# Kernel tuning notes

Measured on AMD Instinct MI355X. Metric: run time of the kernel, lower is better.

The kernel has to match this reference:

```python
import jax, jax.numpy as jnp
import numpy as np

N, E, DIM, H = 50000, 800000, 128, 8
HD = DIM // H  # head dim = 16
EPS = 1e-5


def setup_inputs() -> dict:
    key = jax.random.key(0)
    ks = jax.random.split(key, 12)
    s = 1.0 / np.sqrt(DIM)
    inp = {
        "h": jax.random.normal(ks[0], (N, DIM), jnp.float32),
        "src": jax.random.randint(ks[1], (E,), 0, N, jnp.int32),
        "dst": jax.random.randint(ks[2], (E,), 0, N, jnp.int32),
        "Wq": jax.random.normal(ks[3], (DIM, DIM), jnp.float32) * s,
        "Wk": jax.random.normal(ks[4], (DIM, DIM), jnp.float32) * s,
        "Wv": jax.random.normal(ks[5], (DIM, DIM), jnp.float32) * s,
        "Wo": jax.random.normal(ks[6], (DIM, DIM), jnp.float32) * s,
        "bo": jnp.zeros((DIM,), jnp.float32),
        "bn1_g": jnp.ones((DIM,), jnp.float32),
        "bn1_b": jnp.zeros((DIM,), jnp.float32),
        "bn2_g": jnp.ones((DIM,), jnp.float32),
        "bn2_b": jnp.zeros((DIM,), jnp.float32),
        "W1": jax.random.normal(ks[7], (DIM, 2 * DIM), jnp.float32) * s,
        "b1": jnp.zeros((2 * DIM,), jnp.float32),
        "W2": jax.random.normal(ks[8], (2 * DIM, DIM), jnp.float32) * (1.0 / np.sqrt(2 * DIM)),
        "b2": jnp.zeros((DIM,), jnp.float32),
    }
    return inp


def _batch_norm(x, g, b):
    # BatchNorm1d in training mode: biased batch statistics over the node axis
    mean = jnp.mean(x, axis=0)
    var = jnp.mean((x - mean) ** 2, axis=0)
    return (x - mean) * jax.lax.rsqrt(var + EPS) * g + b


def reference(h, src, dst, Wq, Wk, Wv, Wo, bo, bn1_g, bn1_b, bn2_g, bn2_b, W1, b1, W2, b2):
    n = h.shape[0]
    h_in1 = h
    hn = _batch_norm(h, bn1_g, bn1_b)

    # multi-head graph attention
    Q = (hn @ Wq).reshape(n, H, HD)
    K = (hn @ Wk).reshape(n, H, HD)
    V = (hn @ Wv).reshape(n, H, HD)

    # edge score: sum_d K[src]*Q[dst] / sqrt(HD), clamped to [-5, 5] -> [E, H]
    score = jnp.einsum('ehd,ehd->eh', K[src], Q[dst]) / np.sqrt(HD)
    score = jnp.clip(score, -5.0, 5.0)

    # edge_softmax: normalize over incoming edges of each destination node
    smax = jax.ops.segment_max(score, dst, num_segments=n)  # [N, H]
    a = jnp.exp(score - smax[dst])
    asum = jax.ops.segment_sum(a, dst, num_segments=n)  # [N, H]
    a = a / asum[dst]

    # weighted scatter-sum aggregation of V
    m = V[src] * a[:, :, None]  # [E, H, HD]
    wV = jax.ops.segment_sum(m, dst, num_segments=n).reshape(n, DIM)

    h2 = wV @ Wo + bo
    h2 = h_in1 + h2
    h_in2 = h2
    h3 = _batch_norm(h2, bn2_g, bn2_b)
    h3 = jax.nn.relu(h3 @ W1 + b1) @ W2 + b2
    return h_in2 + h3
```

## Files before the change

### kernel.cpp

```cpp
#include <hip/hip_runtime.h>
#include <hip/hip_bf16.h>

#define NDIM 128
#define NHEAD 8
#define EPSV 1e-5f

#if defined(__has_builtin)
#  if __has_builtin(__builtin_amdgcn_cvt_pk_fp8_f32) && __has_builtin(__builtin_amdgcn_cvt_pk_f32_fp8)
#    define HAVE_FP8 1
#  else
#    define HAVE_FP8 0
#  endif
#else
#  define HAVE_FP8 0
#endif

typedef unsigned short u16;
typedef unsigned char u8;
using bf16x8 = __attribute__((ext_vector_type(8))) short;
using f32x4  = __attribute__((ext_vector_type(4))) float;
using f32x2  = __attribute__((ext_vector_type(2))) float;
using us8    = __attribute__((ext_vector_type(8))) unsigned short;
using us4    = __attribute__((ext_vector_type(4))) unsigned short;

__device__ __forceinline__ u16 f2b(float x){
  union { float f; unsigned u; } v; v.f = x;
  unsigned r = v.u + 0x7FFFu + ((v.u >> 16) & 1u);
  return (u16)(r >> 16);
}
__device__ __forceinline__ float b2f(u16 u){
  union { unsigned u; float f; } v; v.u = ((unsigned)u) << 16; return v.f;
}
__device__ __forceinline__ float blo(unsigned u){
  union { unsigned u; float f; } v; v.u = u << 16; return v.f;
}
__device__ __forceinline__ float bhi(unsigned u){
  union { unsigned u; float f; } v; v.u = u & 0xFFFF0000u; return v.f;
}
__device__ __forceinline__ f32x2 b2f2(unsigned u){
  f32x2 r; r.x = blo(u); r.y = bhi(u); return r;
}

template<int NT, int MT, int KS, int WTLD, int XSTR>
__device__ __forceinline__ void gemm_tiles(const u16* X, const u16* __restrict__ WT,
                                           int lr, int kg, int colbase, f32x4 (&acc)[NT][MT]){
  #pragma unroll
  for (int ks = 0; ks < KS; ks++){
    bf16x8 a[MT];
    #pragma unroll
    for (int m = 0; m < MT; m++)
      a[m] = *(const bf16x8*)(X + (size_t)(m*16 + lr)*XSTR + ks*32 + kg*8);
    #pragma unroll
    for (int n = 0; n < NT; n++){
      int col = colbase + n*16 + lr;
      bf16x8 b = *(const bf16x8*)(WT + (size_t)col*WTLD + ks*32 + kg*8);
      #pragma unroll
      for (int m = 0; m < MT; m++)
        acc[n][m] = __builtin_amdgcn_mfma_f32_16x16x32_bf16(a[m], b, acc[n][m], 0, 0, 0);
    }
  }
}

__device__ __forceinline__ void wconv_tile(const float* __restrict__ W, u16* __restrict__ WT,
                                           int rows, int cols, int tr, int tc, int t){
  __shared__ u16 T[64][66];
  int r0 = tr*64, c0 = tc*64;
  int r = t >> 2, cq = (t & 3) * 16;
  const float* src = W + (size_t)(r0 + r)*cols + c0 + cq;
  #pragma unroll
  for (int j = 0; j < 4; j++){
    float4 v = *(const float4*)(src + 4*j);
    us4 o; o.x = f2b(v.x); o.y = f2b(v.y); o.z = f2b(v.z); o.w = f2b(v.w);
    *(us4*)&T[r][cq + 4*j] = o;
  }
  __syncthreads();
  int c = t >> 2, rq = (t & 3) * 16;
  us8 o0, o1;
  #pragma unroll
  for (int j = 0; j < 8; j++){ o0[j] = T[rq + j][c]; o1[j] = T[rq + 8 + j][c]; }
  u16* dstp = WT + (size_t)(c0 + c)*rows + r0 + rq;
  *(us8*)dstp = o0;
  *(us8*)(dstp + 8) = o1;
}

__global__ __launch_bounds__(256) void k_pro(
    const float* __restrict__ Wq, const float* __restrict__ Wk, const float* __restrict__ Wv,
    const float* __restrict__ Wo, const float* __restrict__ W1, const float* __restrict__ W2,
    u16* __restrict__ wtq, u16* __restrict__ wtk, u16* __restrict__ wtv,
    u16* __restrict__ wto, u16* __restrict__ wt1, u16* __restrict__ wt2,
    const float* __restrict__ h, float* __restrict__ part1,
    const int* __restrict__ dst, int* __restrict__ cntT,
    int nBn, int N, int E, int B, int C){
  __shared__ f32x4 lsS[256], lsQ[256];
  __shared__ int hist[256];
  int b = blockIdx.x, t = threadIdx.x;
  if (b < nBn){
    int qd = t & 31, rl = t >> 5;
    int r0 = b * 128;
    f32x4 s = {0.f,0.f,0.f,0.f}, sq = {0.f,0.f,0.f,0.f};
    for (int r = rl; r < 128; r += 8){
      int row = r0 + r;
      if (row < N){
        f32x4 v = *(const f32x4*)(h + (size_t)row*NDIM + qd*4);
        s += v; sq += v*v;
      }
    }
    lsS[t] = s; lsQ[t] = sq; __syncthreads();
    if (rl < 4){ lsS[t] += lsS[t+128]; lsQ[t] += lsQ[t+128]; } __syncthreads();
    if (rl < 2){ lsS[t] += lsS[t+64];  lsQ[t] += lsQ[t+64];  } __syncthreads();
    if (rl == 0){
      f32x4 S  = lsS[t] + lsS[t+32];
      f32x4 Qv = lsQ[t] + lsQ[t+32];
      *(f32x4*)&part1[(size_t)b*256 + qd*4]       = S;
      *(f32x4*)&part1[(size_t)b*256 + 128 + qd*4] = Qv;
    }
    return;
  }
  b -= nBn;
  if (b < 16){
    const float* Ws[4] = {Wq, Wk, Wv, Wo};
    u16* Ts[4] = {wtq, wtk, wtv, wto};
    int wi = b >> 2, ti = b & 3;
    wconv_tile(Ws[wi], Ts[wi], 128, 128, ti >> 1, ti & 1, t);
    return;
  }
  if (b < 24){
    int ti = b - 16;
    wconv_tile(W1, wt1, 128, 256, ti >> 2, ti & 3, t);
    return;
  }
  if (b < 32){
    int ti = b - 24;
    wconv_tile(W2, wt2, 256, 128, ti & 3, ti >> 2, t);
    return;
  }
  int ci = b - 32;
  if (ci >= C) return;
  hist[t] = 0; __syncthreads();
  int e0 = ci * 4096;
  #pragma unroll
  for (int j = 0; j < 16; j++){
    int e = e0 + t + j*256;
    if (e < E) atomicAdd(&hist[dst[e] >> 8], 1);
  }
  __syncthreads();
  if (t < B) cntT[t*C + ci] = hist[t];
}

__device__ __forceinline__ float reduce_part(const float* __restrict__ part, int nP, int t){
  float a0 = 0.f, a1 = 0.f, a2 = 0.f, a3 = 0.f;
  int i = 0;
  for (; i + 4 <= nP; i += 4){
    a0 += part[(size_t)(i+0)*256 + t];
    a1 += part[(size_t)(i+1)*256 + t];
    a2 += part[(size_t)(i+2)*256 + t];
    a3 += part[(size_t)(i+3)*256 + t];
  }
  for (; i < nP; i++) a0 += part[(size_t)i*256 + t];
  return (a0 + a1) + (a2 + a3);
}

__global__ __launch_bounds__(256) void k_bnf_scan(
    const float* __restrict__ part1, int nBn,
    const float* __restrict__ g, const float* __restrict__ b_,
    float* __restrict__ scsh, int N,
    const int* __restrict__ in, int* __restrict__ bsum, int len){
  __shared__ int ls[256];
  __shared__ float sm[256];
  int t = threadIdx.x, b = blockIdx.x;
  if (b == 0){
    sm[t] = reduce_part(part1, nBn, t);
    __syncthreads();
    if (t < 128){
      float mean = sm[t] / (float)N;
      float var  = sm[128+t] / (float)N - mean*mean;
      float rstd = rsqrtf(var + EPSV);
      float sc = g[t] * rstd;
      scsh[t] = sc; scsh[128+t] = b_[t] - mean*sc;
    }
    return;
  }
  b -= 1;
  int i = b*256 + t;
  ls[t] = (i < len) ? in[i] : 0; __syncthreads();
  for (int off = 128; off > 0; off >>= 1){
    if (t < off) ls[t] += ls[t + off];
    __syncthreads();
  }
  if (t == 0) bsum[b] = ls[0];
}

__global__ __launch_bounds__(256) void k_bn_final(const float* __restrict__ sets,
                                                  const float* __restrict__ g, const float* __restrict__ b,
                                                  float* __restrict__ scsh, int N){
  __shared__ float sm[256];
  int t = threadIdx.x;
  sm[t] = reduce_part(sets, 64, t);
  __syncthreads();
  if (t < 128){
    float mean = sm[t] / (float)N;
    float var  = sm[128+t] / (float)N - mean*mean;
    float rstd = rsqrtf(var + EPSV);
    float sc = g[t] * rstd;
    scsh[t] = sc; scsh[128+t] = b[t] - mean*sc;
  }
}

__global__ __launch_bounds__(256) void k_scan_top(int* __restrict__ bsum, int nb, int* __restrict__ rowptr, int N, int E){
  __shared__ int ls[256];
  int t = threadIdx.x;
  int v = (t < nb) ? bsum[t] : 0; ls[t] = v; __syncthreads();
  for (int off = 1; off < 256; off <<= 1){
    int add = (t >= off) ? ls[t - off] : 0;
    __syncthreads();
    ls[t] += add;
    __syncthreads();
  }
  if (t < nb) bsum[t] = ls[t] - v;
  if (t == 0) rowptr[N] = E;
}

__global__ __launch_bounds__(256) void k_scan_down(const int* __restrict__ in, const int* __restrict__ bsum,
                                                   int* __restrict__ outp, int len){
  __shared__ int ls[256];
  int t = threadIdx.x; int i = blockIdx.x*256 + t;
  int v = (i < len) ? in[i] : 0; ls[t] = v; __syncthreads();
  for (int off = 1; off < 256; off <<= 1){
    int add = (t >= off) ? ls[t - off] : 0;
    __syncthreads();
    ls[t] += add;
    __syncthreads();
  }
  if (i < len) outp[i] = ls[t] - v + bsum[blockIdx.x];
}

__global__ __launch_bounds__(256) void k_finesort(const int2* __restrict__ ebuf, const int* __restrict__ scn,
                                                  int* __restrict__ rowptr, int* __restrict__ csr_src,
                                                  int B, int C, int N, int E){
  __shared__ int ls[256], cur[256];
  int b = blockIdx.x, t = threadIdx.x;
  int base = scn[b*C];
  int end  = (b == B-1) ? E : scn[(b+1)*C];
  int lo = b << 8;
  cur[t] = 0; __syncthreads();
  for (int e = base + t; e < end; e += 256) atomicAdd(&cur[ebuf[e].x - lo], 1);
  __syncthreads();
  int v = cur[t]; ls[t] = v; __syncthreads();
  for (int off = 1; off < 256; off <<= 1){
    int add = (t >= off) ? ls[t - off] : 0;
    __syncthreads();
    ls[t] += add;
    __syncthreads();
  }
  int excl = ls[t] - v;
  __syncthreads();
  cur[t] = excl;
  if (lo + t < N) rowptr[lo + t] = base + excl;
  __syncthreads();
  for (int e = base + t; e < end; e += 256){
    int2 p = ebuf[e];
    int slot = base + atomicAdd(&cur[p.x - lo], 1);
    csr_src[slot] = p.y;
  }
}

__global__ __launch_bounds__(256) void k_qkv_bucket(
    const float* __restrict__ h, const float* __restrict__ scsh,
    const u16* __restrict__ WTq, const u16* __restrict__ WTk, const u16* __restrict__ WTv,
    u16* __restrict__ Q, u16* __restrict__ K, u16* __restrict__ V, int N,
    const int* __restrict__ src, const int* __restrict__ dst,
    const int* __restrict__ scn, int2* __restrict__ ebuf, int B, int C, int E){
  __shared__ u16 hn[32][136];
  __shared__ u16 ob[32][136];
  __shared__ int off[256];
  int b = blockIdx.x, t = threadIdx.x;
  if (b < C){
    off[t] = (t < B) ? scn[t*C + b] : 0;
    __syncthreads();
    int e0 = b * 4096;
    #pragma unroll
    for (int j = 0; j < 16; j++){
      int e = e0 + t + j*256;
      if (e < E){
        int d = dst[e], s = src[e];
        int slot = atomicAdd(&off[d >> 8], 1);
        ebuf[slot] = make_int2(d, s);
      }
    }
    return;
  }
  int r0 = (b - C) * 32;
  int row = t >> 3, c0 = (t & 7) * 16;
  {
    int rr = r0 + row;
    #pragma unroll
    for (int j = 0; j < 4; j++){
      int c = c0 + 4*j;
      float4 v = make_float4(0.f,0.f,0.f,0.f);
      if (rr < N) v = *(const float4*)(h + (size_t)rr*NDIM + c);
      us4 o;
      o.x = f2b(v.x * scsh[c]   + scsh[128+c]);
      o.y = f2b(v.y * scsh[c+1] + scsh[129+c]);
      o.z = f2b(v.z * scsh[c+2] + scsh[130+c]);
      o.w = f2b(v.w * scsh[c+3] + scsh[131+c]);
      *(us4*)&hn[row][c] = o;
    }
  }
  __syncthreads();
  int lane = t & 63, w = t >> 6;
  int lr = lane & 15, kg = lane >> 4;
  f32x4 zero = {0.f,0.f,0.f,0.f};

  #define DO_PASS(WT, OUT, FIRST) { \
    f32x4 acc[2][2]; \
    _Pragma("unroll") for (int n = 0; n < 2; n++) _Pragma("unroll") for (int m = 0; m < 2; m++) acc[n][m] = zero; \
    gemm_tiles<2,2,4,128,136>(&hn[0][0], WT, lr, kg, w*32, acc); \
    if (!FIRST) __syncthreads(); \
    _Pragma("unroll") for (int n = 0; n < 2; n++){ \
      int col = w*32 + n*16 + lr; \
      _Pragma("unroll") for (int m = 0; m < 2; m++) \
        _Pragma("unroll") for (int r = 0; r < 4; r++) \
          ob[m*16 + kg*4 + r][col] = f2b(acc[n][m][r]); \
    } \
    __syncthreads(); \
    if (r0 + row < N){ \
      u16* dp = OUT + (size_t)(r0 + row)*NDIM + c0; \
      *(us8*)dp       = *(const us8*)&ob[row][c0]; \
      *(us8*)(dp + 8) = *(const us8*)&ob[row][c0 + 8]; \
    } }

  DO_PASS(WTq, Q, true)

  {
    f32x4 acc[2][2];
    #pragma unroll
    for (int n = 0; n < 2; n++)
      #pragma unroll
      for (int m = 0; m < 2; m++) acc[n][m] = zero;
    gemm_tiles<2,2,4,128,136>(&hn[0][0], WTk, lr, kg, w*32, acc);
    __syncthreads();
    #pragma unroll
    for (int n = 0; n < 2; n++){
      int col = w*32 + n*16 + lr;
      #pragma unroll
      for (int m = 0; m < 2; m++)
        #pragma unroll
        for (int r = 0; r < 4; r++)
          ob[m*16 + kg*4 + r][col] = f2b(acc[n][m][r]);
    }
    __syncthreads();
    if (r0 + row < N){
#if HAVE_FP8
      u8* dp = (u8*)K + (size_t)(r0 + row)*NDIM + c0;
      unsigned wd[4];
      #pragma unroll
      for (int j = 0; j < 2; j++){
        us8 v = *(const us8*)&ob[row][c0 + 8*j];
        int w0 = __builtin_amdgcn_cvt_pk_fp8_f32(b2f(v[0]), b2f(v[1]), 0, false);
        w0     = __builtin_amdgcn_cvt_pk_fp8_f32(b2f(v[2]), b2f(v[3]), w0, true);
        int w1 = __builtin_amdgcn_cvt_pk_fp8_f32(b2f(v[4]), b2f(v[5]), 0, false);
        w1     = __builtin_amdgcn_cvt_pk_fp8_f32(b2f(v[6]), b2f(v[7]), w1, true);
        wd[2*j] = (unsigned)w0; wd[2*j+1] = (unsigned)w1;
      }
      *(uint4*)dp = make_uint4(wd[0], wd[1], wd[2], wd[3]);
#else
      u16* dp = K + (size_t)(r0 + row)*NDIM + c0;
      *(us8*)dp       = *(const us8*)&ob[row][c0];
      *(us8*)(dp + 8) = *(const us8*)&ob[row][c0 + 8];
#endif
    }
  }

  DO_PASS(WTv, V, false)
  #undef DO_PASS
}

__global__ __launch_bounds__(256) void k_sagg(const int* __restrict__ rowptr, const int* __restrict__ csr_src,
                                              const u16* __restrict__ Q, const u16* __restrict__ K,
                                              const u16* __restrict__ V, u16* __restrict__ wV, int N){
  __shared__ float wx[4][64];
  int w = threadIdx.x >> 6, l = threadIdx.x & 63;
  int n = blockIdx.x*4 + w;
  if (n >= N) return;
  int j8 = l >> 3, hh = l & 7, d0 = l * 2;

  f32x2 qf[8];
  {
    const unsigned* qp = (const unsigned*)(Q + (size_t)n*NDIM + hh*16);
    #pragma unroll
    for (int t = 0; t < 8; t++){
      unsigned u = qp[t];
      qf[t].x = blo(u) * 0.25f;
      qf[t].y = bhi(u) * 0.25f;
    }
  }

  int e0 = rowptr[n], e1 = rowptr[n+1];
  int i0 = __builtin_amdgcn_readfirstlane(e0);
  int deg = e1 - e0;
  int nw  = deg >> 3;
  int rem = deg & 7;

  float ssum_l = 0.f;
  f32x2 a01 = {0.f, 0.f};

#if HAVE_FP8
  const u8* Kb = (const u8*)K;
  uint4 kA, kB;
  #define KLOAD(dst_, sidx) dst_ = *(const uint4*)(Kb + (size_t)(sidx)*NDIM + (hh << 4));
  #define KDOTP(p, kk) { \
    f32x2 p2 = {0.f, 0.f}; \
    p2 += qf[0] * __builtin_amdgcn_cvt_pk_f32_fp8((int)kk.x, false); \
    p2 += qf[1] * __builtin_amdgcn_cvt_pk_f32_fp8((int)kk.x, true); \
    p2 += qf[2] * __builtin_amdgcn_cvt_pk_f32_fp8((int)kk.y, false); \
    p2 += qf[3] * __builtin_amdgcn_cvt_pk_f32_fp8((int)kk.y, true); \
    p2 += qf[4] * __builtin_amdgcn_cvt_pk_f32_fp8((int)kk.z, false); \
    p2 += qf[5] * __builtin_amdgcn_cvt_pk_f32_fp8((int)kk.z, true); \
    p2 += qf[6] * __builtin_amdgcn_cvt_pk_f32_fp8((int)kk.w, false); \
    p2 += qf[7] * __builtin_amdgcn_cvt_pk_f32_fp8((int)kk.w, true); \
    p = p2.x + p2.y; }
#else
  struct krow { uint4 lo, hi; };
  krow kA, kB;
  #define KLOAD(dst_, sidx) { \
    const uint4* kp_ = (const uint4*)(K + (size_t)(sidx)*NDIM + hh*16); \
    dst_.lo = kp_[0]; dst_.hi = kp_[1]; }
  #define KDOTP(p, kk) { \
    f32x2 p2 = {0.f, 0.f}; \
    p2 += qf[0] * b2f2(kk.lo.x); p2 += qf[1] * b2f2(kk.lo.y); \
    p2 += qf[2] * b2f2(kk.lo.z); p2 += qf[3] * b2f2(kk.lo.w); \
    p2 += qf[4] * b2f2(kk.hi.x); p2 += qf[5] * b2f2(kk.hi.y); \
    p2 += qf[6] * b2f2(kk.hi.z); p2 += qf[7] * b2f2(kk.hi.w); \
    p = p2.x + p2.y; }
#endif

  unsigned vvA[8], vvB[8];

  if (nw >= 1){
    int s0=csr_src[i0+0], s1=csr_src[i0+1], s2=csr_src[i0+2], s3=csr_src[i0+3];
    int s4=csr_src[i0+4], s5=csr_src[i0+5], s6=csr_src[i0+6], s7=csr_src[i0+7];
    vvA[0] = *(const unsigned*)(V + (size_t)s0*NDIM + d0);
    vvA[1] = *(const unsigned*)(V + (size_t)s1*NDIM + d0);
    vvA[2] = *(const unsigned*)(V + (size_t)s2*NDIM + d0);
    vvA[3] = *(const unsigned*)(V + (size_t)s3*NDIM + d0);
    vvA[4] = *(const unsigned*)(V + (size_t)s4*NDIM + d0);
    vvA[5] = *(const unsigned*)(V + (size_t)s5*NDIM + d0);
    vvA[6] = *(const unsigned*)(V + (size_t)s6*NDIM + d0);
    vvA[7] = *(const unsigned*)(V + (size_t)s7*NDIM + d0);
    int sidx = csr_src[e0 + j8];
    KLOAD(kA, sidx)
  }

  for (int wi = 0; wi < nw; wi++){
    if (wi + 1 < nw){
      int ib = i0 + wi*8 + 8;
      int s0=csr_src[ib+0], s1=csr_src[ib+1], s2=csr_src[ib+2], s3=csr_src[ib+3];
      int s4=csr_src[ib+4], s5=csr_src[ib+5], s6=csr_src[ib+6], s7=csr_src[ib+7];
      vvB[0] = *(const unsigned*)(V + (size_t)s0*NDIM + d0);
      vvB[1] = *(const unsigned*)(V + (size_t)s1*NDIM + d0);
      vvB[2] = *(const unsigned*)(V + (size_t)s2*NDIM + d0);
      vvB[3] = *(const unsigned*)(V + (size_t)s3*NDIM + d0);
      vvB[4] = *(const unsigned*)(V + (size_t)s4*NDIM + d0);
      vvB[5] = *(const unsigned*)(V + (size_t)s5*NDIM + d0);
      vvB[6] = *(const unsigned*)(V + (size_t)s6*NDIM + d0);
      vvB[7] = *(const unsigned*)(V + (size_t)s7*NDIM + d0);
      int sidx = csr_src[e0 + wi*8 + 8 + j8];
      KLOAD(kB, sidx)
    }
    float p;
    KDOTP(p, kA)
    p = fminf(5.f, fmaxf(-5.f, p));
    float wgt = __expf(p);
    ssum_l += wgt;
    wx[w][hh*8 + j8] = wgt;
    float4 wa = *(const float4*)&wx[w][j8*8];
    float4 wb = *(const float4*)&wx[w][j8*8 + 4];
    a01 += b2f2(vvA[0]) * wa.x;
    a01 += b2f2(vvA[1]) * wa.y;
    a01 += b2f2(vvA[2]) * wa.z;
    a01 += b2f2(vvA[3]) * wa.w;
    a01 += b2f2(vvA[4]) * wb.x;
    a01 += b2f2(vvA[5]) * wb.y;
    a01 += b2f2(vvA[6]) * wb.z;
    a01 += b2f2(vvA[7]) * wb.w;
    if (wi + 1 < nw){
      #pragma unroll
      for (int j = 0; j < 8; j++) vvA[j] = vvB[j];
      kA = kB;
    }
  }

  if (rem > 0){
    int i0t = i0 + nw*8;
    int s[8];
    #pragma unroll
    for (int j = 0; j < 8; j++) s[j] = csr_src[i0t + (j < rem ? j : 0)];
    unsigned vv[8];
    #pragma unroll
    for (int j = 0; j < 8; j++) vv[j] = *(const unsigned*)(V + (size_t)s[j]*NDIM + d0);
    int sidx = csr_src[i0t + (j8 < rem ? j8 : 0)];
#if HAVE_FP8
    uint4 kT;
#else
    krow kT;
#endif
    KLOAD(kT, sidx)
    float p;
    KDOTP(p, kT)
    p = fminf(5.f, fmaxf(-5.f, p));
    float wgt = (j8 < rem) ? __expf(p) : 0.f;
    ssum_l += wgt;
    wx[w][hh*8 + j8] = wgt;
    float4 wa = *(const float4*)&wx[w][j8*8];
    float4 wb = *(const float4*)&wx[w][j8*8 + 4];
    a01 += b2f2(vv[0]) * wa.x;
    a01 += b2f2(vv[1]) * wa.y;
    a01 += b2f2(vv[2]) * wa.z;
    a01 += b2f2(vv[3]) * wa.w;
    a01 += b2f2(vv[4]) * wb.x;
    a01 += b2f2(vv[5]) * wb.y;
    a01 += b2f2(vv[6]) * wb.z;
    a01 += b2f2(vv[7]) * wb.w;
  }
  #undef KLOAD
  #undef KDOTP

  ssum_l += __shfl_xor(ssum_l, 8);
  ssum_l += __shfl_xor(ssum_l, 16);
  ssum_l += __shfl_xor(ssum_l, 32);
  float ssum = __shfl(ssum_l, j8);
  float inv = (e1 > e0) ? 1.f/ssum : 0.f;
  unsigned pk = (unsigned)f2b(a01.x*inv) | (((unsigned)f2b(a01.y*inv)) << 16);
  *(unsigned*)(wV + (size_t)n*NDIM + d0) = pk;
}

__global__ __launch_bounds__(256) void k_h2(const u16* __restrict__ wV, const u16* __restrict__ WTo,
                                            const float* __restrict__ bo, const float* __restrict__ h,
                                            float* __restrict__ h2, float* __restrict__ sets, int N){
  __shared__ u16 tw[32][136];
  __shared__ float ob[32][132];
  int t = threadIdx.x; int r0 = blockIdx.x * 32;
  int row = t >> 3, c0 = (t & 7) * 16;
  {
    int rr = r0 + row;
    us8 z = {0,0,0,0,0,0,0,0};
    const u16* sp = wV + (size_t)rr*NDIM + c0;
    *(us8*)&tw[row][c0]     = (rr < N) ? *(const us8*)sp       : z;
    *(us8*)&tw[row][c0 + 8] = (rr < N) ? *(const us8*)(sp + 8) : z;
  }
  __syncthreads();
  int lane = t & 63, w = t >> 6;
  int lr = lane & 15, kg = lane >> 4;
  f32x4 zero = {0.f,0.f,0.f,0.f};
  f32x4 acc[2][2];
  #pragma unroll
  for (int n = 0; n < 2; n++)
    #pragma unroll
    for (int m = 0; m < 2; m++) acc[n][m] = zero;
  gemm_tiles<2,2,4,128,136>(&tw[0][0], WTo, lr, kg, w*32, acc);
  #pragma unroll
  for (int n = 0; n < 2; n++){
    int col = w*32 + n*16 + lr;
    float bb = bo[col];
    #pragma unroll
    for (int m = 0; m < 2; m++)
      #pragma unroll
      for (int r = 0; r < 4; r++)
        ob[m*16 + kg*4 + r][col] = acc[n][m][r] + bb;
  }
  __syncthreads();
  if (r0 + row < N){
    const float* hp = h  + (size_t)(r0 + row)*NDIM + c0;
    float*       op = h2 + (size_t)(r0 + row)*NDIM + c0;
    #pragma unroll
    for (int j = 0; j < 4; j++){
      float4 hv = *(const float4*)(hp + 4*j);
      float4 o;
      o.x = ob[row][c0 + 4*j]     + hv.x;
      o.y = ob[row][c0 + 4*j + 1] + hv.y;
      o.z = ob[row][c0 + 4*j + 2] + hv.z;
      o.w = ob[row][c0 + 4*j + 3] + hv.w;
      *(float4*)(op + 4*j) = o;
      ob[row][c0 + 4*j]     = o.x;
      ob[row][c0 + 4*j + 1] = o.y;
      ob[row][c0 + 4*j + 2] = o.z;
      ob[row][c0 + 4*j + 3] = o.w;
    }
  } else {
    #pragma unroll
    for (int j = 0; j < 16; j++) ob[row][c0 + j] = 0.f;
  }
  __syncthreads();
  int colx = t & 127, hf = t >> 7;
  float s = 0.f, q = 0.f;
  #pragma unroll
  for (int r = 0; r < 16; r++){ float v = ob[hf*16 + r][colx]; s += v; q += v*v; }
  float* cs = (float*)&tw[0][0];
  cs[hf*256 + colx]       = s;
  cs[hf*256 + 128 + colx] = q;
  __syncthreads();
  if (t < 128){
    float* sp = sets + ((size_t)(blockIdx.x & 63) << 8);
    atomicAdd(&sp[t],       cs[t]       + cs[256 + t]);
    atomicAdd(&sp[128 + t], cs[128 + t] + cs[384 + t]);
  }
}

__global__ __launch_bounds__(256) void k_ffn(const float* __restrict__ h2, const float* __restrict__ scsh,
                                             const u16* __restrict__ WT1, const float* __restrict__ b1,
                                             const u16* __restrict__ WT2, const float* __restrict__ b2,
                                             float* __restrict__ out, int N){
  __shared__ u16 x[32][136];
  __shared__ u16 tt[32][264];
  int t = threadIdx.x; int r0 = blockIdx.x * 32;
  int row = t >> 3, c0 = (t & 7) * 16;
  {
    int rr = r0 + row;
    #pragma unroll
    for (int j = 0; j < 4; j++){
      int c = c0 + 4*j;
      float4 v = make_float4(0.f,0.f,0.f,0.f);
      if (rr < N) v = *(const float4*)(h2 + (size_t)rr*NDIM + c);
      us4 o;
      o.x = f2b(v.x * scsh[c]   + scsh[128+c]);
      o.y = f2b(v.y * scsh[c+1] + scsh[129+c]);
      o.z = f2b(v.z * scsh[c+2] + scsh[130+c]);
      o.w = f2b(v.w * scsh[c+3] + scsh[131+c]);
      *(us4*)&x[row][c] = o;
    }
  }
  __syncthreads();
  int lane = t & 63, w = t >> 6;
  int lr = lane & 15, kg = lane >> 4;
  f32x4 zero = {0.f,0.f,0.f,0.f};
  {
    f32x4 a1[4][2];
    #pragma unroll
    for (int n = 0; n < 4; n++)
      #pragma unroll
      for (int m = 0; m < 2; m++) a1[n][m] = zero;
    gemm_tiles<4,2,4,128,136>(&x[0][0], WT1, lr, kg, w*64, a1);
    #pragma unroll
    for (int n = 0; n < 4; n++){
      int col = w*64 + n*16 + lr;
      float bb = b1[col];
      #pragma unroll
      for (int m = 0; m < 2; m++)
        #pragma unroll
        for (int r = 0; r < 4; r++)
          tt[m*16 + kg*4 + r][col] = f2b(fmaxf(a1[n][m][r] + bb, 0.f));
    }
  }
  __syncthreads();
  f32x4 a2[2][2];
  #pragma unroll
  for (int n = 0; n < 2; n++)
    #pragma unroll
    for (int m = 0; m < 2; m++) a2[n][m] = zero;
  gemm_tiles<2,2,8,256,264>(&tt[0][0], WT2, lr, kg, w*32, a2);
  __syncthreads();
  float* ob2 = (float*)&tt[0][0];
  #pragma unroll
  for (int n = 0; n < 2; n++){
    int col = w*32 + n*16 + lr;
    float bb = b2[col];
    #pragma unroll
    for (int m = 0; m < 2; m++)
      #pragma unroll
      for (int r = 0; r < 4; r++)
        ob2[(m*16 + kg*4 + r)*132 + col] = a2[n][m][r] + bb;
  }
  __syncthreads();
  if (r0 + row < N){
    const float* hp = h2  + (size_t)(r0 + row)*NDIM + c0;
    float*       op = out + (size_t)(r0 + row)*NDIM + c0;
    #pragma unroll
    for (int j = 0; j < 4; j++){
      float4 hv = *(const float4*)(hp + 4*j);
      float4 o;
      o.x = ob2[row*132 + c0 + 4*j]     + hv.x;
      o.y = ob2[row*132 + c0 + 4*j + 1] + hv.y;
      o.z = ob2[row*132 + c0 + 4*j + 2] + hv.z;
      o.w = ob2[row*132 + c0 + 4*j + 3] + hv.w;
      *(float4*)(op + 4*j) = o;
    }
  }
}

extern "C" void kernel_launch(void* const* d_in, const int* in_sizes, int n_in,
                              void* d_out, int out_size, void* d_ws, size_t ws_size,
                              hipStream_t stream) {
  const float* h    = (const float*)d_in[0];
  const int*   src  = (const int*)d_in[1];
  const int*   dst  = (const int*)d_in[2];
  const float* Wq   = (const float*)d_in[3];
  const float* Wk   = (const float*)d_in[4];
  const float* Wv   = (const float*)d_in[5];
  const float* Wo   = (const float*)d_in[6];
  const float* bo   = (const float*)d_in[7];
  const float* bn1g = (const float*)d_in[8];
  const float* bn1b = (const float*)d_in[9];
  const float* bn2g = (const float*)d_in[10];
  const float* bn2b = (const float*)d_in[11];
  const float* W1   = (const float*)d_in[12];
  const float* b1   = (const float*)d_in[13];
  const float* W2   = (const float*)d_in[14];
  const float* b2   = (const float*)d_in[15];
  float* out = (float*)d_out;

  int N = in_sizes[0] / NDIM;
  int E = in_sizes[1];
  size_t fN = (size_t)N * NDIM;

  int B   = (N + 255) >> 8;
  int C   = (E + 4095) >> 12;
  int NB2 = B * C;
  int nb2 = (NB2 + 255) / 256;
  int nBn = (N + 127) / 128;
  int n32 = (N + 31) / 32;

  u16* Q  = (u16*)d_ws;
  u16* K  = Q + fN;
  u16* V  = K + fN;
  u16* wV = Q;
  float* h2   = (float*)(V + fN);
  int2* ebuf  = (int2*)(h2 + fN);
  int* rowptr = (int*)(ebuf + E);
  int* bsum   = rowptr + (N + 1);
  int* cntT   = bsum + 256;
  int* scn    = cntT + NB2;
  int* csr_src= scn + NB2;
  float* part1 = (float*)(csr_src + E);
  float* sets2 = part1 + (size_t)nBn*256;
  float* scsh1 = sets2 + 64*256;
  float* scsh2 = scsh1 + 256;
  u16* wtq = (u16*)(scsh2 + 256);
  u16* wtk = wtq + NDIM*NDIM;
  u16* wtv = wtk + NDIM*NDIM;
  u16* wto = wtv + NDIM*NDIM;
  u16* wt1 = wto + NDIM*NDIM;
  u16* wt2 = wt1 + NDIM*2*NDIM;

  hipMemsetAsync(sets2, 0, 64*256*sizeof(float), stream);

  k_pro<<<nBn + 32 + C, 256, 0, stream>>>(Wq, Wk, Wv, Wo, W1, W2,
                                          wtq, wtk, wtv, wto, wt1, wt2,
                                          h, part1, dst, cntT, nBn, N, E, B, C);
  k_bnf_scan<<<1 + nb2, 256, 0, stream>>>(part1, nBn, bn1g, bn1b, scsh1, N, cntT, bsum, NB2);
  k_scan_top<<<1, 256, 0, stream>>>(bsum, nb2, rowptr, N, E);
  k_scan_down<<<nb2, 256, 0, stream>>>(cntT, bsum, scn, NB2);

  k_qkv_bucket<<<C + n32, 256, 0, stream>>>(h, scsh1, wtq, wtk, wtv, Q, K, V, N,
                                            src, dst, scn, ebuf, B, C, E);
  k_finesort<<<B, 256, 0, stream>>>(ebuf, scn, rowptr, csr_src, B, C, N, E);

  k_sagg<<<(N + 3)/4, 256, 0, stream>>>(rowptr, csr_src, Q, K, V, wV, N);

  k_h2<<<n32, 256, 0, stream>>>(wV, wto, bo, h, h2, sets2, N);
  k_bn_final<<<1, 256, 0, stream>>>(sets2, bn2g, bn2b, scsh2, N);
  k_ffn<<<n32, 256, 0, stream>>>(h2, scsh2, wt1, b1, wt2, b2, out, N);
}
```

Measured before the change: 207.1 us.

## Merge scan kernels, atomically reduce BN1 stats, widen finesort blocks

The BN1 partial sums are now accumulated with atomics into 64 slot sets instead of one row per block, so the first reduction reads 64 rows rather than nBn. The top-level scan and the down-sweep are merged into one kernel in which every block redundantly rescans the block sums, removing one launch. The finesort kernel moves to 1024 threads per block to process each bucket's edges with more parallelism. The cost is float-atomic contention and non-deterministic summation order, plus extra barriers in the wider finesort.

Measured after the change: 176.1 us. 15.0% less time.

```diff
diff --git a/kernel.cpp b/kernel.cpp
--- a/kernel.cpp
+++ b/kernel.cpp
@@ -88,7 +88,7 @@
     const float* __restrict__ Wo, const float* __restrict__ W1, const float* __restrict__ W2,
     u16* __restrict__ wtq, u16* __restrict__ wtk, u16* __restrict__ wtv,
     u16* __restrict__ wto, u16* __restrict__ wt1, u16* __restrict__ wt2,
-    const float* __restrict__ h, float* __restrict__ part1,
+    const float* __restrict__ h, float* __restrict__ sets1,
     const int* __restrict__ dst, int* __restrict__ cntT,
     int nBn, int N, int E, int B, int C){
   __shared__ f32x4 lsS[256], lsQ[256];
@@ -111,8 +111,11 @@
     if (rl == 0){
       f32x4 S  = lsS[t] + lsS[t+32];
       f32x4 Qv = lsQ[t] + lsQ[t+32];
-      *(f32x4*)&part1[(size_t)b*256 + qd*4]       = S;
-      *(f32x4*)&part1[(size_t)b*256 + 128 + qd*4] = Qv;
+      float* sp = sets1 + ((size_t)(b & 63) << 8);
+      atomicAdd(&sp[qd*4+0], S.x); atomicAdd(&sp[qd*4+1], S.y);
+      atomicAdd(&sp[qd*4+2], S.z); atomicAdd(&sp[qd*4+3], S.w);
+      atomicAdd(&sp[128+qd*4+0], Qv.x); atomicAdd(&sp[128+qd*4+1], Qv.y);
+      atomicAdd(&sp[128+qd*4+2], Qv.z); atomicAdd(&sp[128+qd*4+3], Qv.w);
     }
     return;
   }
@@ -161,7 +164,7 @@
 }
 
 __global__ __launch_bounds__(256) void k_bnf_scan(
-    const float* __restrict__ part1, int nBn,
+    const float* __restrict__ sets1,
     const float* __restrict__ g, const float* __restrict__ b_,
     float* __restrict__ scsh, int N,
     const int* __restrict__ in, int* __restrict__ bsum, int len){
@@ -169,7 +172,7 @@
   __shared__ float sm[256];
   int t = threadIdx.x, b = blockIdx.x;
   if (b == 0){
-    sm[t] = reduce_part(part1, nBn, t);
+    sm[t] = reduce_part(sets1, 64, t);
     __syncthreads();
     if (t < 128){
       float mean = sm[t] / (float)N;
@@ -206,58 +209,64 @@
   }
 }
 
-__global__ __launch_bounds__(256) void k_scan_top(int* __restrict__ bsum, int nb, int* __restrict__ rowptr, int N, int E){
-  __shared__ int ls[256];
-  int t = threadIdx.x;
-  int v = (t < nb) ? bsum[t] : 0; ls[t] = v; __syncthreads();
+__global__ __launch_bounds__(256) void k_scan_down2(const int* __restrict__ in, const int* __restrict__ bsum,
+                                                    int nb, int* __restrict__ outp,
+                                                    int* __restrict__ rowptr, int len, int N, int E){
+  __shared__ int ls[256], top[256];
+  int t = threadIdx.x, b = blockIdx.x;
+  int tv = (t < nb) ? bsum[t] : 0;
+  top[t] = tv; __syncthreads();
+  for (int off = 1; off < 256; off <<= 1){
+    int add = (t >= off) ? top[t - off] : 0;
+    __syncthreads();
+    top[t] += add;
+    __syncthreads();
+  }
+  int base = (b > 0) ? top[b - 1] : 0;
+  int i = b*256 + t;
+  int v = (i < len) ? in[i] : 0;
+  ls[t] = v; __syncthreads();
   for (int off = 1; off < 256; off <<= 1){
     int add = (t >= off) ? ls[t - off] : 0;
     __syncthreads();
     ls[t] += add;
     __syncthreads();
   }
-  if (t < nb) bsum[t] = ls[t] - v;
-  if (t == 0) rowptr[N] = E;
-}
-
-__global__ __launch_bounds__(256) void k_scan_down(const int* __restrict__ in, const int* __restrict__ bsum,
-                                                   int* __restrict__ outp, int len){
-  __shared__ int ls[256];
-  int t = threadIdx.x; int i = blockIdx.x*256 + t;
-  int v = (i < len) ? in[i] : 0; ls[t] = v; __syncthreads();
-  for (int off = 1; off < 256; off <<= 1){
-    int add = (t >= off) ? ls[t - off] : 0;
-    __syncthreads();
-    ls[t] += add;
-    __syncthreads();
-  }
-  if (i < len) outp[i] = ls[t] - v + bsum[blockIdx.x];
-}
-
-__global__ __launch_bounds__(256) void k_finesort(const int2* __restrict__ ebuf, const int* __restrict__ scn,
-                                                  int* __restrict__ rowptr, int* __restrict__ csr_src,
-                                                  int B, int C, int N, int E){
+  if (i < len) outp[i] = ls[t] - v + base;
+  if (b == 0 && t == 0) rowptr[N] = E;
+}
+
+__global__ __launch_bounds__(1024) void k_finesort(const int2* __restrict__ ebuf, const int* __restrict__ scn,
+                                                   int* __restrict__ rowptr, int* __restrict__ csr_src,
+                                                   int B, int C, int N, int E){
   __shared__ int ls[256], cur[256];
   int b = blockIdx.x, t = threadIdx.x;
   int base = scn[b*C];
   int end  = (b == B-1) ? E : scn[(b+1)*C];
   int lo = b << 8;
-  cur[t] = 0; __syncthreads();
-  for (int e = base + t; e < end; e += 256) atomicAdd(&cur[ebuf[e].x - lo], 1);
-  __syncthreads();
-  int v = cur[t]; ls[t] = v; __syncthreads();
+  if (t < 256) cur[t] = 0;
+  __syncthreads();
+  for (int e = base + t; e < end; e += 1024) atomicAdd(&cur[ebuf[e].x - lo], 1);
+  __syncthreads();
+  int cnt_t = 0;
+  if (t < 256){ cnt_t = cur[t]; ls[t] = cnt_t; }
+  __syncthreads();
   for (int off = 1; off < 256; off <<= 1){
-    int add = (t >= off) ? ls[t - off] : 0;
-    __syncthreads();
-    ls[t] += add;
-    __syncthreads();
-  }
-  int excl = ls[t] - v;
-  __syncthreads();
-  cur[t] = excl;
-  if (lo + t < N) rowptr[lo + t] = base + excl;
-  __syncthreads();
-  for (int e = base + t; e < end; e += 256){
+    int add = 0;
+    if (t < 256 && t >= off) add = ls[t - off];
+    __syncthreads();
+    if (t < 256) ls[t] += add;
+    __syncthreads();
+  }
+  int excl_t = 0;
+  if (t < 256){
+    excl_t = ls[t] - cnt_t;
+    if (lo + t < N) rowptr[lo + t] = base + excl_t;
+  }
+  __syncthreads();
+  if (t < 256) cur[t] = excl_t;
+  __syncthreads();
+  for (int e = base + t; e < end; e += 1024){
     int2 p = ebuf[e];
     int slot = base + atomicAdd(&cur[p.x - lo], 1);
     csr_src[slot] = p.y;
@@ -730,8 +739,8 @@
   int* cntT   = bsum + 256;
   int* scn    = cntT + NB2;
   int* csr_src= scn + NB2;
-  float* part1 = (float*)(csr_src + E);
-  float* sets2 = part1 + (size_t)nBn*256;
+  float* sets1 = (float*)(csr_src + E);
+  float* sets2 = sets1 + 64*256;
   float* scsh1 = sets2 + 64*256;
   float* scsh2 = scsh1 + 256;
   u16* wtq = (u16*)(scsh2 + 256);
@@ -741,18 +750,17 @@
   u16* wt1 = wto + NDIM*NDIM;
   u16* wt2 = wt1 + NDIM*2*NDIM;
 
-  hipMemsetAsync(sets2, 0, 64*256*sizeof(float), stream);
+  hipMemsetAsync(sets1, 0, 2*64*256*sizeof(float), stream);
 
   k_pro<<<nBn + 32 + C, 256, 0, stream>>>(Wq, Wk, Wv, Wo, W1, W2,
                                           wtq, wtk, wtv, wto, wt1, wt2,
-                                          h, part1, dst, cntT, nBn, N, E, B, C);
-  k_bnf_scan<<<1 + nb2, 256, 0, stream>>>(part1, nBn, bn1g, bn1b, scsh1, N, cntT, bsum, NB2);
-  k_scan_top<<<1, 256, 0, stream>>>(bsum, nb2, rowptr, N, E);
-  k_scan_down<<<nb2, 256, 0, stream>>>(cntT, bsum, scn, NB2);
+                                          h, sets1, dst, cntT, nBn, N, E, B, C);
+  k_bnf_scan<<<1 + nb2, 256, 0, stream>>>(sets1, bn1g, bn1b, scsh1, N, cntT, bsum, NB2);
+  k_scan_down2<<<nb2, 256, 0, stream>>>(cntT, bsum, nb2, scn, rowptr, NB2, N, E);
 
   k_qkv_bucket<<<C + n32, 256, 0, stream>>>(h, scsh1, wtq, wtk, wtv, Q, K, V, N,
                                             src, dst, scn, ebuf, B, C, E);
-  k_finesort<<<B, 256, 0, stream>>>(ebuf, scn, rowptr, csr_src, B, C, N, E);
+  k_finesort<<<B, 1024, 0, stream>>>(ebuf, scn, rowptr, csr_src, B, C, N, E);
 
   k_sagg<<<(N + 3)/4, 256, 0, stream>>>(rowptr, csr_src, Q, K, V, wV, N);
 
```
